# Kernel optimization log

Measured on AMD Instinct MI355X. Metric: run time of the kernel, lower is better.

## Reference

```python
import jax, jax.numpy as jnp
import numpy as np

N = 100000   # nodes
E = 640000   # edges
D = 128      # feature dim
G = 512      # graphs in the batch


def setup_inputs() -> dict:
    key = jax.random.key(0)
    ks = jax.random.split(key, 6)
    x = jax.random.normal(ks[0], (N, D), dtype=jnp.float32)
    edge_index = jax.random.randint(ks[1], (2, E), 0, N, dtype=jnp.int32)
    batch = jnp.sort(jax.random.randint(ks[2], (N,), 0, G, dtype=jnp.int32))
    scale = 1.0 / np.sqrt(D)
    W0 = jax.random.normal(ks[3], (D, D), dtype=jnp.float32) * scale
    W1 = jax.random.normal(ks[4], (D, D), dtype=jnp.float32) * scale
    W2 = jax.random.normal(ks[5], (D, D), dtype=jnp.float32) * scale
    return {"x": x, "edge_index": edge_index, "batch": batch,
            "W0": W0, "W1": W1, "W2": W2}


def gcn_conv(x, W, row, col, n):
    """GCNConv (bias=False): x' = D^-1/2 (A + I) D^-1/2 (x @ W).
    row/col already include self-loops."""
    xw = x @ W                                              # [N, D]
    deg = jax.ops.segment_sum(jnp.ones_like(col, dtype=x.dtype), col,
                              num_segments=n)               # [N]
    dinv = jnp.where(deg > 0, jax.lax.rsqrt(deg), 0.0)
    norm = dinv[row] * dinv[col]                            # [E+N]
    msgs = norm[:, None] * xw[row]                          # gather + scale
    return jax.ops.segment_sum(msgs, col, num_segments=n)   # scatter-add


def reference(x, edge_index, batch, W0, W1, W2):
    n = x.shape[0]
    loops = jnp.arange(n, dtype=edge_index.dtype)
    row = jnp.concatenate([edge_index[0], loops])
    col = jnp.concatenate([edge_index[1], loops])
    # conv_layers[:-1] (no activation between them in forward)
    x = gcn_conv(x, W0, row, col, n)
    x = gcn_conv(x, W1, row, col, n)
    x = jax.nn.leaky_relu(x, negative_slope=0.01)
    x = gcn_conv(x, W2, row, col, n)
    # global_add_pool over graph ids
    return jax.ops.segment_sum(x, batch, num_segments=G)    # [G, D]
```

## Files before the change

### kernel.cpp

```cpp
#include <hip/hip_runtime.h>
#include <hip/hip_bf16.h>

#define FEAT 128

typedef unsigned int uint32;
typedef unsigned short ushort16;
typedef __attribute__((ext_vector_type(8))) short short8;
typedef __attribute__((ext_vector_type(4))) float v4f;
typedef __attribute__((ext_vector_type(2))) float f32x2;

__device__ __forceinline__ ushort16 f2bf(float f) {
    uint32 u = __float_as_uint(f);
    u += 0x7fffu + ((u >> 16) & 1u);
    return (ushort16)(u >> 16);
}
__device__ __forceinline__ float bflo(uint32 u) { return __uint_as_float(u << 16); }
__device__ __forceinline__ float bfhi(uint32 u) { return __uint_as_float(u & 0xffff0000u); }
__device__ __forceinline__ f32x2 up2(uint32 u) { return (f32x2){bflo(u), bfhi(u)}; }

__global__ __launch_bounds__(256) void hydra_kernel(const int* __restrict__ col,
                                                    int* __restrict__ counts,
                                                    const float* __restrict__ W0,
                                                    const float* __restrict__ W1,
                                                    ushort16* __restrict__ W01t,
                                                    float* __restrict__ Pbuf,
                                                    int histBlocks, int E) {
    int b = blockIdx.x;
    int t = threadIdx.x;
    if (b < histBlocks) {
        int id = b * 256 + t;
        if (id * 4 + 3 < E) {
            int4 c4 = *(const int4*)(col + id * 4);
            atomicAdd(&counts[c4.x], 1);
            atomicAdd(&counts[c4.y], 1);
            atomicAdd(&counts[c4.z], 1);
            atomicAdd(&counts[c4.w], 1);
        } else {
            for (int e = id * 4; e < E; e++) atomicAdd(&counts[col[e]], 1);
        }
    } else if (b < histBlocks + 64) {
        __shared__ float sW0[2][FEAT];
        int wb = b - histBlocks;
        int lk = t >> 7;
        int ncol = t & 127;
        int k = wb * 2 + lk;
        sW0[lk][ncol] = W0[(size_t)k * FEAT + ncol];
        __syncthreads();
        float acc = 0.f;
#pragma unroll 4
        for (int j = 0; j < FEAT; j++)
            acc += sW0[lk][j] * W1[(size_t)j * FEAT + ncol];
        W01t[(size_t)ncol * FEAT + k] = f2bf(acc);
    } else {
        int zb = b - histBlocks - 64;
        float4 z = make_float4(0.f, 0.f, 0.f, 0.f);
        float* p = Pbuf + (size_t)zb * 2048 + t * 8;
        *(float4*)p = z;
        *(float4*)(p + 4) = z;
    }
}

__global__ __launch_bounds__(256) void scan_part(const int* __restrict__ counts,
                                                 int* __restrict__ bsum, int n) {
    __shared__ int s[256];
    int base = blockIdx.x * 1024;
    int t = threadIdx.x;
    int v = 0;
#pragma unroll
    for (int i = 0; i < 4; i++) {
        int idx = base + t * 4 + i;
        if (idx < n) v += counts[idx];
    }
    s[t] = v;
    __syncthreads();
    for (int o = 128; o > 0; o >>= 1) {
        if (t < o) s[t] += s[t + o];
        __syncthreads();
    }
    if (t == 0) bsum[blockIdx.x] = s[0];
}

__global__ __launch_bounds__(256) void scan_final(const int* __restrict__ counts,
                                                  const int* __restrict__ bsum,
                                                  int* __restrict__ off, int* __restrict__ nxt,
                                                  float* __restrict__ dinv, int n, int nb) {
    __shared__ int s[256];
    __shared__ int sb[128];
    int base = blockIdx.x * 1024;
    int t = threadIdx.x;
    if (t < nb) sb[t] = bsum[t];
    int c[4];
    int sum = 0;
#pragma unroll
    for (int i = 0; i < 4; i++) {
        int idx = base + t * 4 + i;
        c[i] = (idx < n) ? counts[idx] : 0;
        sum += c[i];
    }
    int v0 = sum;
    s[t] = sum;
    __syncthreads();
    for (int o = 1; o < 256; o <<= 1) {
        int v = (t >= o) ? s[t - o] : 0;
        __syncthreads();
        s[t] += v;
        __syncthreads();
    }
    int blockBase = 0;
    for (int j = 0; j < blockIdx.x; j++) blockBase += sb[j];
    int excl = s[t] - v0 + blockBase;
#pragma unroll
    for (int i = 0; i < 4; i++) {
        int idx = base + t * 4 + i;
        if (idx < n) {
            off[idx] = excl;
            nxt[idx] = excl;
            dinv[idx] = rsqrtf((float)(c[i] + 1));
        }
        excl += c[i];
    }
    if (blockIdx.x == gridDim.x - 1 && t == 255) off[n] = excl;
}

__global__ __launch_bounds__(256) void gemmfill_kernel(const float* __restrict__ A,
                                                       const ushort16* __restrict__ Wt,
                                                       ushort16* __restrict__ Ch, int n,
                                                       const int* __restrict__ row,
                                                       const int* __restrict__ col,
                                                       int* __restrict__ nxt,
                                                       int* __restrict__ srcArr, int E) {
    const int b = blockIdx.x;
    const int r7 = b % 7;
    const int g7 = b / 7;
    const int t = threadIdx.x;

    if (r7 >= 2) {
        int fb = g7 * 5 + (r7 - 2);
        int e = fb * 256 + t;
        if (e < E) {
            int c = col[e], r = row[e];
            int p = atomicAdd(&nxt[c], 1);
            __builtin_nontemporal_store(r, &srcArr[p]);
        }
        return;
    }

    const int gb = g7 * 2 + r7;
    const int GEMM_BLOCKS = 1024;
    const int w = t >> 6;
    const int lane = t & 63;
    const int quad = lane >> 4;
    const int l16 = lane & 15;
    const int colBase = (w & 1) * 64;

    short8 wf[4][4];
#pragma unroll
    for (int ct = 0; ct < 4; ct++) {
        const ushort16* wp = Wt + (size_t)(colBase + ct * 16 + l16) * FEAT + quad * 8;
#pragma unroll
        for (int ks = 0; ks < 4; ks++) wf[ct][ks] = *(const short8*)(wp + ks * 32);
    }

    const int nTiles = (n + 15) >> 4;
    const int tStride = GEMM_BLOCKS * 2;
    int tile = gb * 2 + (w >> 1);
    if (tile >= nTiles) return;

    auto loadA = [&](int tl, short8 (&a)[4]) {
        const int rowi = tl * 16 + l16;
        if (rowi < n) {
#pragma unroll
            for (int ks = 0; ks < 4; ks++) {
                const float* ap = A + (size_t)rowi * FEAT + quad * 8 + ks * 32;
                float4 f0 = *(const float4*)ap;
                float4 f1 = *(const float4*)(ap + 4);
                short8 v;
                v[0] = f2bf(f0.x); v[1] = f2bf(f0.y); v[2] = f2bf(f0.z); v[3] = f2bf(f0.w);
                v[4] = f2bf(f1.x); v[5] = f2bf(f1.y); v[6] = f2bf(f1.z); v[7] = f2bf(f1.w);
                a[ks] = v;
            }
        } else {
#pragma unroll
            for (int ks = 0; ks < 4; ks++) a[ks] = (short8)0;
        }
    };

    short8 aCur[4];
    loadA(tile, aCur);

    while (tile < nTiles) {
        const int nextTile = tile + tStride;
        short8 aNxt[4];
        if (nextTile < nTiles) loadA(nextTile, aNxt);

        v4f acc[4];
#pragma unroll
        for (int ct = 0; ct < 4; ct++) acc[ct] = (v4f)0.f;
#pragma unroll
        for (int ct = 0; ct < 4; ct++)
#pragma unroll
            for (int ks = 0; ks < 4; ks++)
                acc[ct] = __builtin_amdgcn_mfma_f32_16x16x32_bf16(wf[ct][ks], aCur[ks], acc[ct], 0, 0, 0);

        const int rowi = tile * 16 + l16;
        if (rowi < n) {
#pragma unroll
            for (int ct = 0; ct < 4; ct++) {
                uint2 o;
                o.x = (uint32)f2bf(acc[ct][0]) | ((uint32)f2bf(acc[ct][1]) << 16);
                o.y = (uint32)f2bf(acc[ct][2]) | ((uint32)f2bf(acc[ct][3]) << 16);
                *(uint2*)(Ch + (size_t)rowi * FEAT + colBase + ct * 16 + quad * 4) = o;
            }
        }

        tile = nextTile;
#pragma unroll
        for (int ks = 0; ks < 4; ks++) aCur[ks] = aNxt[ks];
    }
}

__global__ __launch_bounds__(256) void gather_kernel(const int* __restrict__ off,
                                                     const int* __restrict__ srcArr,
                                                     const float* __restrict__ dinv,
                                                     const ushort16* __restrict__ XWh,
                                                     ushort16* __restrict__ Hh, int n,
                                                     int leaky) {
    int node = blockIdx.x * 4 + (threadIdx.x >> 6);
    if (node >= n) return;
    int lane = threadIdx.x & 63;
    int grp = lane >> 4;
    int l16 = lane & 15;
    float dc = dinv[node];
    const uint4* table = (const uint4*)XWh;

    f32x2 acc[4];
    if (grp == 0) {
        uint4 v = table[(size_t)node * 16 + l16];
        f32x2 w0 = (f32x2){dc * dc, dc * dc};
        acc[0] = w0 * up2(v.x);
        acc[1] = w0 * up2(v.y);
        acc[2] = w0 * up2(v.z);
        acc[3] = w0 * up2(v.w);
    } else {
#pragma unroll
        for (int j = 0; j < 4; j++) acc[j] = (f32x2){0.f, 0.f};
    }

    int s = off[node], e = off[node + 1];
    int i = s + grp;
    for (; i + 4 < e; i += 8) {
        int r0 = srcArr[i];
        int r1 = srcArr[i + 4];
        uint4 u0 = table[(size_t)r0 * 16 + l16];
        uint4 u1 = table[(size_t)r1 * 16 + l16];
        float f0 = dc * dinv[r0];
        float f1 = dc * dinv[r1];
        f32x2 n0 = (f32x2){f0, f0};
        f32x2 n1 = (f32x2){f1, f1};
        acc[0] += n0 * up2(u0.x);
        acc[1] += n0 * up2(u0.y);
        acc[2] += n0 * up2(u0.z);
        acc[3] += n0 * up2(u0.w);
        acc[0] += n1 * up2(u1.x);
        acc[1] += n1 * up2(u1.y);
        acc[2] += n1 * up2(u1.z);
        acc[3] += n1 * up2(u1.w);
    }
    if (i < e) {
        int r0 = srcArr[i];
        uint4 u0 = table[(size_t)r0 * 16 + l16];
        float f0 = dc * dinv[r0];
        f32x2 n0 = (f32x2){f0, f0};
        acc[0] += n0 * up2(u0.x);
        acc[1] += n0 * up2(u0.y);
        acc[2] += n0 * up2(u0.z);
        acc[3] += n0 * up2(u0.w);
    }

    float b[8] = {acc[0].x, acc[0].y, acc[1].x, acc[1].y,
                  acc[2].x, acc[2].y, acc[3].x, acc[3].y};
#pragma unroll
    for (int j = 0; j < 8; j++) {
        b[j] += __shfl_xor(b[j], 16);
        b[j] += __shfl_xor(b[j], 32);
    }

    if (grp == 0) {
        if (leaky) {
#pragma unroll
            for (int j = 0; j < 8; j++) b[j] = (b[j] >= 0.f) ? b[j] : 0.01f * b[j];
        }
        uint4 o;
        o.x = (uint32)f2bf(b[0]) | ((uint32)f2bf(b[1]) << 16);
        o.y = (uint32)f2bf(b[2]) | ((uint32)f2bf(b[3]) << 16);
        o.z = (uint32)f2bf(b[4]) | ((uint32)f2bf(b[5]) << 16);
        o.w = (uint32)f2bf(b[6]) | ((uint32)f2bf(b[7]) << 16);
        *(uint4*)(Hh + (size_t)node * FEAT + l16 * 8) = o;
    }
}

__global__ __launch_bounds__(128) void pool_kernel(const ushort16* __restrict__ H,
                                                   const int* __restrict__ batch,
                                                   float* __restrict__ P, int n) {
    int t = threadIdx.x;
    int i0 = blockIdx.x * 64;
    if (i0 >= n) return;
    int i1 = min(i0 + 64, n);
    float acc = 0.f;
    int g = batch[i0];
    for (int i = i0; i < i1; i++) {
        int b = batch[i];
        if (b != g) {
            atomicAdd(&P[(size_t)g * FEAT + t], acc);
            acc = 0.f;
            g = b;
        }
        uint32 u = (uint32)(unsigned short)H[(size_t)i * FEAT + t];
        acc += __uint_as_float(u << 16);
    }
    atomicAdd(&P[(size_t)g * FEAT + t], acc);
}

__global__ __launch_bounds__(128) void pgemm_kernel(const float* __restrict__ P,
                                                    const float* __restrict__ W2,
                                                    float* __restrict__ out) {
    __shared__ float sP[FEAT];
    const int g = blockIdx.x;
    const int t = threadIdx.x;
    sP[t] = P[(size_t)g * FEAT + t];
    __syncthreads();
    float o = 0.f;
#pragma unroll 4
    for (int k = 0; k < FEAT; k++) o += sP[k] * W2[(size_t)k * FEAT + t];
    out[(size_t)g * FEAT + t] = o;
}

extern "C" void kernel_launch(void* const* d_in, const int* in_sizes, int n_in,
                              void* d_out, int out_size, void* d_ws, size_t ws_size,
                              hipStream_t stream) {
    const float* x = (const float*)d_in[0];
    const int* ei = (const int*)d_in[1];
    const int* batch = (const int*)d_in[2];
    const float* W0 = (const float*)d_in[3];
    const float* W1 = (const float*)d_in[4];
    const float* W2 = (const float*)d_in[5];
    float* out = (float*)d_out;

    const int N = in_sizes[0] / FEAT;
    const int E = in_sizes[1] / 2;
    const int G = out_size / FEAT;

    const int* rowI = ei;
    const int* colI = ei + E;

    char* ws = (char*)d_ws;
    auto take = [&](size_t bytes) {
        char* p = ws;
        ws += (bytes + 15) & ~(size_t)15;
        return p;
    };
    int* counts    = (int*)take((size_t)N * 4);
    int* off       = (int*)take((size_t)(N + 1) * 4);
    int* nxt       = (int*)take((size_t)N * 4);
    float* dinv    = (float*)take((size_t)N * 4);
    int* bsum      = (int*)take(128 * 4);
    int* srcArr    = (int*)take((size_t)E * 4);
    ushort16* W01t = (ushort16*)take((size_t)16384 * 2);
    float* Pbuf    = (float*)take((size_t)G * FEAT * 4);
    ushort16* bufA = (ushort16*)take((size_t)N * FEAT * 2);
    ushort16* bufB = (ushort16*)take((size_t)N * FEAT * 2);

    const int nb = (N + 1023) / 1024;

    hipMemsetAsync(counts, 0, (size_t)N * 4, stream);
    const int histBlocks = (E + 1023) / 1024;
    hydra_kernel<<<histBlocks + 64 + 32, 256, 0, stream>>>(
        colI, counts, W0, W1, W01t, Pbuf, histBlocks, E);

    scan_part<<<nb, 256, 0, stream>>>(counts, bsum, N);
    scan_final<<<nb, 256, 0, stream>>>(counts, bsum, off, nxt, dinv, N, nb);

    gemmfill_kernel<<<512 * 7, 256, 0, stream>>>(x, W01t, bufA, N,
                                                 rowI, colI, nxt, srcArr, E);

    const int gatBlocks = (N + 3) / 4;
    gather_kernel<<<gatBlocks, 256, 0, stream>>>(off, srcArr, dinv, bufA, bufB, N, 0);
    gather_kernel<<<gatBlocks, 256, 0, stream>>>(off, srcArr, dinv, bufB, bufA, N, 1);
    gather_kernel<<<gatBlocks, 256, 0, stream>>>(off, srcArr, dinv, bufA, bufB, N, 0);
    pool_kernel<<<(N + 63) / 64, 128, 0, stream>>>(bufB, batch, Pbuf, N);
    pgemm_kernel<<<G, 128, 0, stream>>>(Pbuf, W2, out);
}
```

Baseline: 340.5 us.

## Split feature GEMM across histogram and fill kernels, replace memset with kernel zeroing

The dense x@W01 GEMM is split into two halves of the tile range. The first half is co-scheduled with the degree histogram atomics and the second with the CSR fill scatter, so latency-bound atomic work overlaps with MFMA compute. The counts memset moves into the precompute kernel, and the pool kernel uses 32-node chunks instead of 64 for more parallelism. This relies on the hardcoded tile split 3125/6250 matching N, and it adds a kernel launch boundary dependency between W01t and the histogram kernel.

Result: faster. 332.1 us (-2.5%).

```diff
diff --git a/kernel.cpp b/kernel.cpp
--- a/kernel.cpp
+++ b/kernel.cpp
@@ -18,29 +18,98 @@
 __device__ __forceinline__ float bfhi(uint32 u) { return __uint_as_float(u & 0xffff0000u); }
 __device__ __forceinline__ f32x2 up2(uint32 u) { return (f32x2){bflo(u), bfhi(u)}; }
 
-__global__ __launch_bounds__(256) void hydra_kernel(const int* __restrict__ col,
-                                                    int* __restrict__ counts,
-                                                    const float* __restrict__ W0,
-                                                    const float* __restrict__ W1,
-                                                    ushort16* __restrict__ W01t,
-                                                    float* __restrict__ Pbuf,
-                                                    int histBlocks, int E) {
+__device__ __forceinline__ void gemm_body(const float* __restrict__ A,
+                                          const ushort16* __restrict__ Wt,
+                                          ushort16* __restrict__ Ch, int n,
+                                          int pairId, int pairStride,
+                                          int tile0, int tile1, int t) {
+    const int w = t >> 6;
+    const int lane = t & 63;
+    const int quad = lane >> 4;
+    const int l16 = lane & 15;
+    const int colBase = (w & 1) * 64;
+
+    short8 wf[4][4];
+#pragma unroll
+    for (int ct = 0; ct < 4; ct++) {
+        const ushort16* wp = Wt + (size_t)(colBase + ct * 16 + l16) * FEAT + quad * 8;
+#pragma unroll
+        for (int ks = 0; ks < 4; ks++) wf[ct][ks] = *(const short8*)(wp + ks * 32);
+    }
+
+    int tile = tile0 + pairId;
+    if (tile >= tile1) return;
+
+    auto loadA = [&](int tl, short8 (&a)[4]) {
+        const int rowi = tl * 16 + l16;
+        if (rowi < n) {
+#pragma unroll
+            for (int ks = 0; ks < 4; ks++) {
+                const float* ap = A + (size_t)rowi * FEAT + quad * 8 + ks * 32;
+                float4 f0 = *(const float4*)ap;
+                float4 f1 = *(const float4*)(ap + 4);
+                short8 v;
+                v[0] = f2bf(f0.x); v[1] = f2bf(f0.y); v[2] = f2bf(f0.z); v[3] = f2bf(f0.w);
+                v[4] = f2bf(f1.x); v[5] = f2bf(f1.y); v[6] = f2bf(f1.z); v[7] = f2bf(f1.w);
+                a[ks] = v;
+            }
+        } else {
+#pragma unroll
+            for (int ks = 0; ks < 4; ks++) a[ks] = (short8)0;
+        }
+    };
+
+    short8 aCur[4];
+    loadA(tile, aCur);
+
+    while (tile < tile1) {
+        const int nextTile = tile + pairStride;
+        short8 aNxt[4];
+        if (nextTile < tile1) loadA(nextTile, aNxt);
+
+        v4f acc[4];
+#pragma unroll
+        for (int ct = 0; ct < 4; ct++) acc[ct] = (v4f)0.f;
+#pragma unroll
+        for (int ct = 0; ct < 4; ct++)
+#pragma unroll
+            for (int ks = 0; ks < 4; ks++)
+                acc[ct] = __builtin_amdgcn_mfma_f32_16x16x32_bf16(wf[ct][ks], aCur[ks], acc[ct], 0, 0, 0);
+
+        const int rowi = tile * 16 + l16;
+        if (rowi < n) {
+#pragma unroll
+            for (int ct = 0; ct < 4; ct++) {
+                uint2 o;
+                o.x = (uint32)f2bf(acc[ct][0]) | ((uint32)f2bf(acc[ct][1]) << 16);
+                o.y = (uint32)f2bf(acc[ct][2]) | ((uint32)f2bf(acc[ct][3]) << 16);
+                *(uint2*)(Ch + (size_t)rowi * FEAT + colBase + ct * 16 + quad * 4) = o;
+            }
+        }
+
+        tile = nextTile;
+#pragma unroll
+        for (int ks = 0; ks < 4; ks++) aCur[ks] = aNxt[ks];
+    }
+}
+
+__global__ __launch_bounds__(256) void pre_kernel(int* __restrict__ counts, int n,
+                                                  const float* __restrict__ W0,
+                                                  const float* __restrict__ W1,
+                                                  ushort16* __restrict__ W01t,
+                                                  float* __restrict__ Pbuf) {
     int b = blockIdx.x;
     int t = threadIdx.x;
-    if (b < histBlocks) {
-        int id = b * 256 + t;
-        if (id * 4 + 3 < E) {
-            int4 c4 = *(const int4*)(col + id * 4);
-            atomicAdd(&counts[c4.x], 1);
-            atomicAdd(&counts[c4.y], 1);
-            atomicAdd(&counts[c4.z], 1);
-            atomicAdd(&counts[c4.w], 1);
+    if (b < 100) {
+        int idx = (b * 256 + t) * 4;
+        if (idx + 3 < n) {
+            *(int4*)(counts + idx) = make_int4(0, 0, 0, 0);
         } else {
-            for (int e = id * 4; e < E; e++) atomicAdd(&counts[col[e]], 1);
-        }
-    } else if (b < histBlocks + 64) {
+            for (int i = idx; i < n; i++) counts[i] = 0;
+        }
+    } else if (b < 164) {
         __shared__ float sW0[2][FEAT];
-        int wb = b - histBlocks;
+        int wb = b - 100;
         int lk = t >> 7;
         int ncol = t & 127;
         int k = wb * 2 + lk;
@@ -52,12 +121,39 @@
             acc += sW0[lk][j] * W1[(size_t)j * FEAT + ncol];
         W01t[(size_t)ncol * FEAT + k] = f2bf(acc);
     } else {
-        int zb = b - histBlocks - 64;
+        int zb = b - 164;
         float4 z = make_float4(0.f, 0.f, 0.f, 0.f);
         float* p = Pbuf + (size_t)zb * 2048 + t * 8;
         *(float4*)p = z;
         *(float4*)(p + 4) = z;
     }
+}
+
+__global__ __launch_bounds__(256) void histgemmA_kernel(const int* __restrict__ col,
+                                                        int* __restrict__ counts, int E,
+                                                        const float* __restrict__ A,
+                                                        const ushort16* __restrict__ Wt,
+                                                        ushort16* __restrict__ Ch, int n) {
+    const int b = blockIdx.x;
+    const int r9 = b % 9;
+    const int g9 = b / 9;
+    const int t = threadIdx.x;
+    if (r9 >= 4) {
+        int hb = g9 * 5 + (r9 - 4);
+        int id = hb * 256 + t;
+        if (id * 4 + 3 < E) {
+            int4 c4 = *(const int4*)(col + id * 4);
+            atomicAdd(&counts[c4.x], 1);
+            atomicAdd(&counts[c4.y], 1);
+            atomicAdd(&counts[c4.z], 1);
+            atomicAdd(&counts[c4.w], 1);
+        } else {
+            for (int e = id * 4; e < E; e++) atomicAdd(&counts[col[e]], 1);
+        }
+        return;
+    }
+    int gb = g9 * 4 + r9;
+    gemm_body(A, Wt, Ch, n, gb * 2 + ((t >> 6) >> 1), 1024, 0, 3125, t);
 }
 
 __global__ __launch_bounds__(256) void scan_part(const int* __restrict__ counts,
@@ -122,18 +218,17 @@
     if (blockIdx.x == gridDim.x - 1 && t == 255) off[n] = excl;
 }
 
-__global__ __launch_bounds__(256) void gemmfill_kernel(const float* __restrict__ A,
-                                                       const ushort16* __restrict__ Wt,
-                                                       ushort16* __restrict__ Ch, int n,
-                                                       const int* __restrict__ row,
-                                                       const int* __restrict__ col,
-                                                       int* __restrict__ nxt,
-                                                       int* __restrict__ srcArr, int E) {
+__global__ __launch_bounds__(256) void fillgemmB_kernel(const float* __restrict__ A,
+                                                        const ushort16* __restrict__ Wt,
+                                                        ushort16* __restrict__ Ch, int n,
+                                                        const int* __restrict__ row,
+                                                        const int* __restrict__ col,
+                                                        int* __restrict__ nxt,
+                                                        int* __restrict__ srcArr, int E) {
     const int b = blockIdx.x;
     const int r7 = b % 7;
     const int g7 = b / 7;
     const int t = threadIdx.x;
-
     if (r7 >= 2) {
         int fb = g7 * 5 + (r7 - 2);
         int e = fb * 256 + t;
@@ -144,79 +239,8 @@
         }
         return;
     }
-
-    const int gb = g7 * 2 + r7;
-    const int GEMM_BLOCKS = 1024;
-    const int w = t >> 6;
-    const int lane = t & 63;
-    const int quad = lane >> 4;
-    const int l16 = lane & 15;
-    const int colBase = (w & 1) * 64;
-
-    short8 wf[4][4];
-#pragma unroll
-    for (int ct = 0; ct < 4; ct++) {
-        const ushort16* wp = Wt + (size_t)(colBase + ct * 16 + l16) * FEAT + quad * 8;
-#pragma unroll
-        for (int ks = 0; ks < 4; ks++) wf[ct][ks] = *(const short8*)(wp + ks * 32);
-    }
-
-    const int nTiles = (n + 15) >> 4;
-    const int tStride = GEMM_BLOCKS * 2;
-    int tile = gb * 2 + (w >> 1);
-    if (tile >= nTiles) return;
-
-    auto loadA = [&](int tl, short8 (&a)[4]) {
-        const int rowi = tl * 16 + l16;
-        if (rowi < n) {
-#pragma unroll
-            for (int ks = 0; ks < 4; ks++) {
-                const float* ap = A + (size_t)rowi * FEAT + quad * 8 + ks * 32;
-                float4 f0 = *(const float4*)ap;
-                float4 f1 = *(const float4*)(ap + 4);
-                short8 v;
-                v[0] = f2bf(f0.x); v[1] = f2bf(f0.y); v[2] = f2bf(f0.z); v[3] = f2bf(f0.w);
-                v[4] = f2bf(f1.x); v[5] = f2bf(f1.y); v[6] = f2bf(f1.z); v[7] = f2bf(f1.w);
-                a[ks] = v;
-            }
-        } else {
-#pragma unroll
-            for (int ks = 0; ks < 4; ks++) a[ks] = (short8)0;
-        }
-    };
-
-    short8 aCur[4];
-    loadA(tile, aCur);
-
-    while (tile < nTiles) {
-        const int nextTile = tile + tStride;
-        short8 aNxt[4];
-        if (nextTile < nTiles) loadA(nextTile, aNxt);
-
-        v4f acc[4];
-#pragma unroll
-        for (int ct = 0; ct < 4; ct++) acc[ct] = (v4f)0.f;
-#pragma unroll
-        for (int ct = 0; ct < 4; ct++)
-#pragma unroll
-            for (int ks = 0; ks < 4; ks++)
-                acc[ct] = __builtin_amdgcn_mfma_f32_16x16x32_bf16(wf[ct][ks], aCur[ks], acc[ct], 0, 0, 0);
-
-        const int rowi = tile * 16 + l16;
-        if (rowi < n) {
-#pragma unroll
-            for (int ct = 0; ct < 4; ct++) {
-                uint2 o;
-                o.x = (uint32)f2bf(acc[ct][0]) | ((uint32)f2bf(acc[ct][1]) << 16);
-                o.y = (uint32)f2bf(acc[ct][2]) | ((uint32)f2bf(acc[ct][3]) << 16);
-                *(uint2*)(Ch + (size_t)rowi * FEAT + colBase + ct * 16 + quad * 4) = o;
-            }
-        }
-
-        tile = nextTile;
-#pragma unroll
-        for (int ks = 0; ks < 4; ks++) aCur[ks] = aNxt[ks];
-    }
+    int gb = g7 * 2 + r7;
+    gemm_body(A, Wt, Ch, n, gb * 2 + ((t >> 6) >> 1), 2048, 3125, 6250, t);
 }
 
 __global__ __launch_bounds__(256) void gather_kernel(const int* __restrict__ off,
@@ -303,9 +327,9 @@
                                                    const int* __restrict__ batch,
                                                    float* __restrict__ P, int n) {
     int t = threadIdx.x;
-    int i0 = blockIdx.x * 64;
+    int i0 = blockIdx.x * 32;
     if (i0 >= n) return;
-    int i1 = min(i0 + 64, n);
+    int i1 = min(i0 + 32, n);
     float acc = 0.f;
     int g = batch[i0];
     for (int i = i0; i < i1; i++) {
@@ -372,21 +396,20 @@
 
     const int nb = (N + 1023) / 1024;
 
-    hipMemsetAsync(counts, 0, (size_t)N * 4, stream);
-    const int histBlocks = (E + 1023) / 1024;
-    hydra_kernel<<<histBlocks + 64 + 32, 256, 0, stream>>>(
-        colI, counts, W0, W1, W01t, Pbuf, histBlocks, E);
+    pre_kernel<<<196, 256, 0, stream>>>(counts, N, W0, W1, W01t, Pbuf);
+
+    histgemmA_kernel<<<128 * 9, 256, 0, stream>>>(colI, counts, E, x, W01t, bufA, N);
 
     scan_part<<<nb, 256, 0, stream>>>(counts, bsum, N);
     scan_final<<<nb, 256, 0, stream>>>(counts, bsum, off, nxt, dinv, N, nb);
 
-    gemmfill_kernel<<<512 * 7, 256, 0, stream>>>(x, W01t, bufA, N,
-                                                 rowI, colI, nxt, srcArr, E);
+    fillgemmB_kernel<<<512 * 7, 256, 0, stream>>>(x, W01t, bufA, N,
+                                                  rowI, colI, nxt, srcArr, E);
 
     const int gatBlocks = (N + 3) / 4;
     gather_kernel<<<gatBlocks, 256, 0, stream>>>(off, srcArr, dinv, bufA, bufB, N, 0);
     gather_kernel<<<gatBlocks, 256, 0, stream>>>(off, srcArr, dinv, bufB, bufA, N, 1);
     gather_kernel<<<gatBlocks, 256, 0, stream>>>(off, srcArr, dinv, bufA, bufB, N, 0);
-    pool_kernel<<<(N + 63) / 64, 128, 0, stream>>>(bufB, batch, Pbuf, N);
+    pool_kernel<<<(N + 31) / 32, 128, 0, stream>>>(bufB, batch, Pbuf, N);
     pgemm_kernel<<<G, 128, 0, stream>>>(Pbuf, W2, out);
 }
```
